# Kernel optimization log

Hardware: AMD Instinct MI355X
Metric: run time of the kernel (lower is better)

The kernel has to match this reference:

```python
import jax, jax.numpy as jnp
import numpy as np

B, N, D_IN, D_OUT = 4, 2048, 1024, 1024


def setup_inputs() -> dict:
    key = jax.random.key(0)
    k0, k1, k2, k3 = jax.random.split(key, 4)
    x = jax.random.normal(k0, (B, N, D_IN), dtype=jnp.float32)
    # torch Linear weight is [out, in]; store transposed [in, out] for x @ W
    W_query = jax.random.normal(k1, (D_IN, D_OUT), dtype=jnp.float32) * (D_IN ** -0.5)
    W_key = jax.random.normal(k2, (D_IN, D_OUT), dtype=jnp.float32) * (D_IN ** -0.5)
    W_value = jax.random.normal(k3, (D_IN, D_OUT), dtype=jnp.float32) * (D_IN ** -0.5)
    return {"x": x, "W_query": W_query, "W_key": W_key, "W_value": W_value}


def reference(x, W_query, W_key, W_value):
    # x: [B, N, D_IN]
    num_tokens = x.shape[1]
    embed_dim = x.shape[2]  # NB: original scales by INPUT embed dim
    q = jnp.einsum('bnd,de->bne', x, W_query)  # [B, N, D_OUT]
    k = jnp.einsum('bnd,de->bne', x, W_key)
    v = jnp.einsum('bnd,de->bne', x, W_value)
    scores = jnp.einsum('bqe,bke->bqk', q, k)  # [B, N, N]
    idx = jnp.arange(num_tokens)
    causal_mask = idx[None, :] > idx[:, None]  # True above diagonal
    scores = jnp.where(causal_mask[None, :, :], -jnp.inf, scores)
    scale = jnp.asarray(embed_dim, scores.dtype) ** 0.5
    attn = jax.nn.softmax(scores / scale, axis=-1)  # dropout p=0 (eval)
    context = jnp.einsum('bqk,bke->bqe', attn, v)  # [B, N, D_OUT]
    return context
```

## Files before the change

kernel.cpp:

```cpp
#include <hip/hip_runtime.h>


typedef __attribute__((ext_vector_type(8))) _Float16 half8;
typedef __attribute__((ext_vector_type(4))) _Float16 half4v;
typedef __attribute__((ext_vector_type(4))) float floatx4;

#define AS1 __attribute__((address_space(1)))
#define AS3 __attribute__((address_space(3)))

__device__ __forceinline__ void load16_lds(void* lds, const void* g) {
  __builtin_amdgcn_global_load_lds((AS1 void*)g, (AS3 void*)lds, 16, 0, 0);
}

__global__ __launch_bounds__(256)
void prep(const float* __restrict__ in, _Float16* __restrict__ out,
          const float* __restrict__ W0, const float* __restrict__ W1,
          const float* __restrict__ W2, _Float16* __restrict__ Wt) {
  const int bid = blockIdx.x;
  if (bid < 8192) {
    const int i = (bid * 256 + threadIdx.x) << 2;
    float4 v = *(const float4*)(in + i);
    half4v o = { (_Float16)v.x, (_Float16)v.y, (_Float16)v.z, (_Float16)v.w };
    *(half4v*)(out + i) = o;
  } else {
    const int t = bid - 8192;
    const int bz = t >> 10;
    const int rem = t & 1023;
    const int bx = rem & 31, by = rem >> 5;
    const float* W = bz == 0 ? W0 : (bz == 1 ? W1 : W2);
    _Float16* o = Wt + (long long)bz * 1048576;
    __shared__ _Float16 tl[32][33];
    const int tx = threadIdx.x & 31, ty = threadIdx.x >> 5;
    const int n0 = bx << 5, k0 = by << 5;
#pragma unroll
    for (int i = 0; i < 4; ++i)
      tl[ty + i * 8][tx] = (_Float16)W[(long long)(k0 + ty + i * 8) * 1024 + n0 + tx];
    __syncthreads();
#pragma unroll
    for (int i = 0; i < 4; ++i)
      o[(long long)(n0 + ty + i * 8) * 1024 + k0 + tx] = tl[tx][ty + i * 8];
  }
}

__global__ __launch_bounds__(256)
void gemm_qkv(const _Float16* __restrict__ A, const _Float16* __restrict__ B,
              _Float16* __restrict__ Q, _Float16* __restrict__ Kh,
              _Float16* __restrict__ Vt) {
  const int lid = blockIdx.x + 24 * blockIdx.y;
  const int swz = (lid & 7) * 192 + (lid >> 3);
  const int bm = swz / 24, bn = swz % 24;

  const _Float16* Ab = A + (long long)bm * 128 * 1024;
  const _Float16* Bb = B + (long long)bn * 128 * 1024;

  __shared__ _Float16 As[128][64];
  __shared__ _Float16 Bs[128][64];

  const int tid = threadIdx.x;
  const int wave = tid >> 6, lane = tid & 63;
  const int quad = lane >> 4, lr = lane & 15;
  const int wm = (wave >> 1) << 6, wn = (wave & 1) << 6;
  const int srow = lane >> 3;
  const int goff = ((lane & 7) ^ srow) << 3;

  floatx4 acc[4][4] = {};
  const _Float16* ga = Ab + (long long)(wave * 8 + srow) * 1024 + goff;
  const _Float16* gb = Bb + (long long)(wave * 8 + srow) * 1024 + goff;

  for (int k0 = 0; k0 < 1024; k0 += 64) {
    __syncthreads();
#pragma unroll
    for (int c = 0; c < 4; ++c) {
      load16_lds(&As[wave * 8 + 32 * c][0], ga + c * 32 * 1024);
      load16_lds(&Bs[wave * 8 + 32 * c][0], gb + c * 32 * 1024);
    }
    ga += 64; gb += 64;
    __syncthreads();

#pragma unroll
    for (int kk = 0; kk < 2; ++kk) {
      half8 af[4], bf[4];
#pragma unroll
      for (int i = 0; i < 4; ++i) {
        const int ra = wm + (i << 4) + lr;
        const int rb = wn + (i << 4) + lr;
        af[i] = *(const half8*)&As[ra][(((kk << 2) + quad) ^ (ra & 7)) << 3];
        bf[i] = *(const half8*)&Bs[rb][(((kk << 2) + quad) ^ (rb & 7)) << 3];
      }
#pragma unroll
      for (int i = 0; i < 4; ++i)
#pragma unroll
        for (int j = 0; j < 4; ++j)
          acc[i][j] = __builtin_amdgcn_mfma_f32_16x16x32_f16(af[i], bf[j], acc[i][j], 0, 0, 0);
    }
  }

  const int colb = bn * 128 + wn + lr;
  const int rowb = bm * 128 + wm + (quad << 2);

  if (bn < 16) {
    _Float16* C = (bn < 8) ? Q : Kh;
    const int cb = colb & 1023;
#pragma unroll
    for (int i = 0; i < 4; ++i)
#pragma unroll
      for (int j = 0; j < 4; ++j)
#pragma unroll
        for (int r = 0; r < 4; ++r)
          C[(long long)(rowb + (i << 4) + r) * 1024 + cb + (j << 4)] =
              (_Float16)acc[i][j][r];
  } else {
    const int b = rowb >> 11;
    const int tb = rowb & 2047;
#pragma unroll
    for (int i = 0; i < 4; ++i) {
      const int tok = tb + (i << 4);
#pragma unroll
      for (int j = 0; j < 4; ++j) {
        const int d = (colb & 1023) + (j << 4);
        half4v v = { (_Float16)acc[i][j][0], (_Float16)acc[i][j][1],
                     (_Float16)acc[i][j][2], (_Float16)acc[i][j][3] };
        *(half4v*)&Vt[(long long)b * 2097152 + (long long)d * 2048 + tok] = v;
      }
    }
  }
}

__global__ __launch_bounds__(256)
void gemm_s_exp(const _Float16* __restrict__ Q, const _Float16* __restrict__ Kh,
                _Float16* __restrict__ P, float* __restrict__ M,
                float* __restrict__ L) {
  int t = (blockIdx.x & 7) * 17 + (blockIdx.x >> 3);
  int bm = 0;
  for (;;) { const int c = bm + 1; if (t < c) break; t -= c; ++bm; }
  const int bn = t;
  const int bz = blockIdx.y;

  const _Float16* Ab = Q  + (long long)bz * 2097152 + (long long)bm * 128 * 1024;
  const _Float16* Bb = Kh + (long long)bz * 2097152 + (long long)bn * 128 * 1024;

  __shared__ _Float16 As[128][64];
  __shared__ _Float16 Bs[128][64];
  __shared__ float sm_m[2][2][64];
  __shared__ float sm_s[2][2][64];

  const int tid = threadIdx.x;
  const int wave = tid >> 6, lane = tid & 63;
  const int quad = lane >> 4, lr = lane & 15;
  const int wm = (wave >> 1) << 6, wn = (wave & 1) << 6;
  const int wm1 = wave >> 1, wn1 = wave & 1;
  const int srow = lane >> 3;
  const int schunk = lane & 7;
  const int goff = (schunk ^ srow) << 3;

  floatx4 acc[4][4] = {};
  const _Float16* ga = Ab + (long long)(wave * 8 + srow) * 1024 + goff;
  const _Float16* gb = Bb + (long long)(wave * 8 + srow) * 1024 + goff;

  half8 pa[4], pb[4];
#pragma unroll
  for (int c = 0; c < 4; ++c) {
    pa[c] = *(const half8*)(ga + c * 32 * 1024);
    pb[c] = *(const half8*)(gb + c * 32 * 1024);
  }

  for (int it = 0; it < 16; ++it) {
    __syncthreads();
#pragma unroll
    for (int c = 0; c < 4; ++c) {
      *(half8*)&As[wave * 8 + 32 * c + srow][schunk << 3] = pa[c];
      *(half8*)&Bs[wave * 8 + 32 * c + srow][schunk << 3] = pb[c];
    }
    __syncthreads();
    if (it + 1 < 16) {
      const int k1 = (it + 1) << 6;
#pragma unroll
      for (int c = 0; c < 4; ++c) {
        pa[c] = *(const half8*)(ga + c * 32 * 1024 + k1);
        pb[c] = *(const half8*)(gb + c * 32 * 1024 + k1);
      }
    }

#pragma unroll
    for (int kk = 0; kk < 2; ++kk) {
      half8 af[4], bf[4];
#pragma unroll
      for (int i = 0; i < 4; ++i) {
        const int ra = wm + (i << 4) + lr;
        const int rb = wn + (i << 4) + lr;
        af[i] = *(const half8*)&As[ra][(((kk << 2) + quad) ^ (ra & 7)) << 3];
        bf[i] = *(const half8*)&Bs[rb][(((kk << 2) + quad) ^ (rb & 7)) << 3];
      }
#pragma unroll
      for (int i = 0; i < 4; ++i)
#pragma unroll
        for (int j = 0; j < 4; ++j)
          acc[i][j] = __builtin_amdgcn_mfma_f32_16x16x32_f16(af[i], bf[j], acc[i][j], 0, 0, 0);
    }
  }

  const int colb = bn * 128 + wn + lr;
  const int rowb = bm * 128 + wm + (quad << 2);
  _Float16* Pb = P + (long long)bz * 4194304;
  const float scl = 0.03125f;

  float mx[4][4], rs[4][4];
#pragma unroll
  for (int i = 0; i < 4; ++i)
#pragma unroll
    for (int r = 0; r < 4; ++r) { mx[i][r] = -3.0e38f; rs[i][r] = 0.f; }

#pragma unroll
  for (int i = 0; i < 4; ++i)
#pragma unroll
    for (int j = 0; j < 4; ++j)
#pragma unroll
      for (int r = 0; r < 4; ++r) {
        const int qr = rowb + (i << 4) + r;
        const int kcol = colb + (j << 4);
        if (kcol <= qr) mx[i][r] = fmaxf(mx[i][r], acc[i][j][r] * scl);
      }
#pragma unroll
  for (int i = 0; i < 4; ++i)
#pragma unroll
    for (int r = 0; r < 4; ++r) {
#pragma unroll
      for (int off = 1; off < 16; off <<= 1)
        mx[i][r] = fmaxf(mx[i][r], __shfl_xor(mx[i][r], off));
    }

  if (lr == 0) {
#pragma unroll
    for (int i = 0; i < 4; ++i)
#pragma unroll
      for (int r = 0; r < 4; ++r)
        sm_m[wm1][wn1][(i << 4) + (quad << 2) + r] = mx[i][r];
  }
  __syncthreads();
  float mt[4][4];
#pragma unroll
  for (int i = 0; i < 4; ++i)
#pragma unroll
    for (int r = 0; r < 4; ++r)
      mt[i][r] = fmaxf(mx[i][r], sm_m[wm1][wn1 ^ 1][(i << 4) + (quad << 2) + r]);

#pragma unroll
  for (int i = 0; i < 4; ++i)
#pragma unroll
    for (int j = 0; j < 4; ++j)
#pragma unroll
      for (int r = 0; r < 4; ++r) {
        const int qr = rowb + (i << 4) + r;
        const int kcol = colb + (j << 4);
        const float pv =
            (kcol <= qr) ? __expf(acc[i][j][r] * scl - mt[i][r]) : 0.f;
        Pb[(long long)qr * 2048 + kcol] = (_Float16)pv;
        rs[i][r] += pv;
      }

#pragma unroll
  for (int i = 0; i < 4; ++i)
#pragma unroll
    for (int r = 0; r < 4; ++r) {
#pragma unroll
      for (int off = 1; off < 16; off <<= 1)
        rs[i][r] += __shfl_xor(rs[i][r], off);
    }

  if (lr == 0) {
#pragma unroll
    for (int i = 0; i < 4; ++i)
#pragma unroll
      for (int r = 0; r < 4; ++r)
        sm_s[wm1][wn1][(i << 4) + (quad << 2) + r] = rs[i][r];
  }
  __syncthreads();
  if (wn1 == 0 && lr == 0) {
    float* Mb = M + ((long long)bz * 16 + bn) * 2048;
    float* Lb = L + ((long long)bz * 16 + bn) * 2048;
#pragma unroll
    for (int i = 0; i < 4; ++i)
#pragma unroll
      for (int r = 0; r < 4; ++r) {
        const int lrow = (i << 4) + (quad << 2) + r;
        const int row = rowb + (i << 4) + r;
        Mb[row] = mt[i][r];
        Lb[row] = rs[i][r] + sm_s[wm1][1][lrow];
      }
  }
}

__global__ __launch_bounds__(256)
void combine(const float* __restrict__ M, const float* __restrict__ L,
             float* __restrict__ F, float* __restrict__ lg) {
  const int idx = blockIdx.x * 256 + threadIdx.x;
  const int bz = idx >> 11, row = idx & 2047;
  const int nt = (row >> 7) + 1;
  const float* Mb = M + (long long)bz * 32768;
  const float* Lb = L + (long long)bz * 32768;
  float* Fb = F + (long long)bz * 32768;

  float mg = -3.0e38f;
  for (int t = 0; t < nt; ++t) mg = fmaxf(mg, Mb[t * 2048 + row]);
  float s = 0.f;
  for (int t = 0; t < nt; ++t) {
    const float f = __expf(Mb[t * 2048 + row] - mg);
    Fb[t * 2048 + row] = f;
    s += f * Lb[t * 2048 + row];
  }
  lg[bz * 2048 + row] = s;
}

__global__ __launch_bounds__(256)
void gemm_pv(const _Float16* __restrict__ P, const _Float16* __restrict__ Vt,
             const float* __restrict__ F, const float* __restrict__ lg,
             float* __restrict__ out) {
  const int lid = blockIdx.x + (blockIdx.y << 3) + (blockIdx.z << 7);
  const int xcd = lid & 7, slot = lid >> 3;
  const int dn = slot & 7;
  const int p = slot >> 3;
  const int bz = p & 3;
  const int bm = (p >> 2) ? xcd : (15 - xcd);
  const int niter = 2 * (bm + 1);

  const _Float16* Ab = P  + (long long)bz * 4194304 + (long long)bm * 128 * 2048;
  const _Float16* Bb = Vt + (long long)bz * 2097152 + (long long)dn * 128 * 2048;
  const float* Fb = F + (long long)bz * 32768 + (long long)bm * 128;

  __shared__ _Float16 As[128][64];
  __shared__ _Float16 Bs[128][64];

  const int tid = threadIdx.x;
  const int wave = tid >> 6, lane = tid & 63;
  const int quad = lane >> 4, lr = lane & 15;
  const int wm = (wave >> 1) << 6, wn = (wave & 1) << 6;
  const int srow = lane >> 3;
  const int schunk = lane & 7;
  const int goff = (schunk ^ srow) << 3;
  const int lrow0 = wave * 8 + srow;

  floatx4 acc[4][4] = {};
  const _Float16* ga = Ab + (long long)lrow0 * 2048 + goff;
  const _Float16* gb = Bb + (long long)lrow0 * 2048 + goff;

  half8 pa[4], pb[4];
  float fr[4];
#pragma unroll
  for (int c = 0; c < 4; ++c) {
    pa[c] = *(const half8*)(ga + (long long)c * 32 * 2048);
    pb[c] = *(const half8*)(gb + (long long)c * 32 * 2048);
    fr[c] = Fb[lrow0 + 32 * c];
  }

  for (int it = 0; it < niter; ++it) {
    __syncthreads();
#pragma unroll
    for (int c = 0; c < 4; ++c) {
      *(half8*)&As[wave * 8 + 32 * c + srow][schunk << 3] =
          pa[c] * (_Float16)fr[c];
      *(half8*)&Bs[wave * 8 + 32 * c + srow][schunk << 3] = pb[c];
    }
    __syncthreads();
    if (it + 1 < niter) {
      const int k1 = (it + 1) << 6;
      const int kt1 = (it + 1) >> 1;
#pragma unroll
      for (int c = 0; c < 4; ++c) {
        pa[c] = *(const half8*)(ga + (long long)c * 32 * 2048 + k1);
        pb[c] = *(const half8*)(gb + (long long)c * 32 * 2048 + k1);
        fr[c] = Fb[kt1 * 2048 + lrow0 + 32 * c];
      }
    }

#pragma unroll
    for (int kk = 0; kk < 2; ++kk) {
      half8 af[4], bf[4];
#pragma unroll
      for (int i = 0; i < 4; ++i) {
        const int ra = wm + (i << 4) + lr;
        const int rb = wn + (i << 4) + lr;
        af[i] = *(const half8*)&As[ra][(((kk << 2) + quad) ^ (ra & 7)) << 3];
        bf[i] = *(const half8*)&Bs[rb][(((kk << 2) + quad) ^ (rb & 7)) << 3];
      }
#pragma unroll
      for (int i = 0; i < 4; ++i)
#pragma unroll
        for (int j = 0; j < 4; ++j)
          acc[i][j] = __builtin_amdgcn_mfma_f32_16x16x32_f16(af[i], bf[j], acc[i][j], 0, 0, 0);
    }
  }

  const int colb = dn * 128 + wn + lr;
  const int rowb = bm * 128 + wm + (quad << 2);
  const float* lb = lg + bz * 2048;
  float* Cb = out + (long long)bz * 2097152;

  float linv[4][4];
#pragma unroll
  for (int i = 0; i < 4; ++i)
#pragma unroll
    for (int r = 0; r < 4; ++r)
      linv[i][r] = 1.0f / lb[rowb + (i << 4) + r];

#pragma unroll
  for (int i = 0; i < 4; ++i)
#pragma unroll
    for (int j = 0; j < 4; ++j)
#pragma unroll
      for (int r = 0; r < 4; ++r)
        Cb[(long long)(rowb + (i << 4) + r) * 1024 + colb + (j << 4)] =
            acc[i][j][r] * linv[i][r];
}


extern "C" void kernel_launch(void* const* d_in, const int* in_sizes, int n_in,
                              void* d_out, int out_size, void* d_ws, size_t ws_size,
                              hipStream_t stream) {
  const float* x  = (const float*)d_in[0];
  const float* Wq = (const float*)d_in[1];
  const float* Wk = (const float*)d_in[2];
  const float* Wv = (const float*)d_in[3];
  float* out = (float*)d_out;

  char* ws = (char*)d_ws;
  _Float16* xh = (_Float16*)(ws);
  _Float16* Wt = (_Float16*)(ws + 16777216);
  _Float16* Q  = (_Float16*)(ws + 23068672);
  _Float16* Kh = (_Float16*)(ws + 39845888);
  _Float16* Vt = (_Float16*)(ws + 56623104);
  _Float16* P  = (_Float16*)(ws + 73400320);
  float*    M  = (float*)   (ws + 106954752);
  float*    L  = (float*)   (ws + 107479040);
  float*    F  = (float*)   (ws + 108003328);
  float*    lg = (float*)   (ws + 108527616);

  prep<<<11264, 256, 0, stream>>>(x, xh, Wq, Wk, Wv, Wt);

  gemm_qkv<<<dim3(24, 64), 256, 0, stream>>>(xh, Wt, Q, Kh, Vt);

  gemm_s_exp<<<dim3(136, 4), 256, 0, stream>>>(Q, Kh, P, M, L);

  combine<<<32, 256, 0, stream>>>(M, L, F, lg);

  gemm_pv<<<dim3(8, 16, 4), 256, 0, stream>>>(P, Vt, F, lg, out);
}
```

Baseline: 254.7 us.

## Fuse softmax combine into PV GEMM, swap operands for vectorized stores

```diff
diff --git a/kernel.cpp b/kernel.cpp
--- a/kernel.cpp
+++ b/kernel.cpp
@@ -46,10 +46,7 @@
 void gemm_qkv(const _Float16* __restrict__ A, const _Float16* __restrict__ B,
               _Float16* __restrict__ Q, _Float16* __restrict__ Kh,
               _Float16* __restrict__ Vt) {
-  const int lid = blockIdx.x + 24 * blockIdx.y;
-  const int swz = (lid & 7) * 192 + (lid >> 3);
-  const int bm = swz / 24, bn = swz % 24;
-
+  const int bm = blockIdx.y, bn = blockIdx.x;
   const _Float16* Ab = A + (long long)bm * 128 * 1024;
   const _Float16* Bb = B + (long long)bn * 128 * 1024;
 
@@ -291,44 +288,27 @@
 }
 
 __global__ __launch_bounds__(256)
-void combine(const float* __restrict__ M, const float* __restrict__ L,
-             float* __restrict__ F, float* __restrict__ lg) {
-  const int idx = blockIdx.x * 256 + threadIdx.x;
-  const int bz = idx >> 11, row = idx & 2047;
-  const int nt = (row >> 7) + 1;
-  const float* Mb = M + (long long)bz * 32768;
-  const float* Lb = L + (long long)bz * 32768;
-  float* Fb = F + (long long)bz * 32768;
-
-  float mg = -3.0e38f;
-  for (int t = 0; t < nt; ++t) mg = fmaxf(mg, Mb[t * 2048 + row]);
-  float s = 0.f;
-  for (int t = 0; t < nt; ++t) {
-    const float f = __expf(Mb[t * 2048 + row] - mg);
-    Fb[t * 2048 + row] = f;
-    s += f * Lb[t * 2048 + row];
-  }
-  lg[bz * 2048 + row] = s;
-}
-
-__global__ __launch_bounds__(256)
 void gemm_pv(const _Float16* __restrict__ P, const _Float16* __restrict__ Vt,
-             const float* __restrict__ F, const float* __restrict__ lg,
+             const float* __restrict__ M, const float* __restrict__ L,
              float* __restrict__ out) {
   const int lid = blockIdx.x + (blockIdx.y << 3) + (blockIdx.z << 7);
-  const int xcd = lid & 7, slot = lid >> 3;
-  const int dn = slot & 7;
-  const int p = slot >> 3;
-  const int bz = p & 3;
-  const int bm = (p >> 2) ? xcd : (15 - xcd);
+  const int xcd = lid & 7;
+  const int s = lid >> 3;
+  const int p = s >> 4;
+  const int dnl = (s >> 2) & 3;
+  const int bz = s & 3;
+  const int bmg = xcd >> 1, dng = xcd & 1;
+  const int bm = (p < 2) ? (15 - 2 * bmg - p) : (2 * bmg + (3 - p));
+  const int dn = dng * 4 + dnl;
   const int niter = 2 * (bm + 1);
 
-  const _Float16* Ab = P  + (long long)bz * 4194304 + (long long)bm * 128 * 2048;
-  const _Float16* Bb = Vt + (long long)bz * 2097152 + (long long)dn * 128 * 2048;
-  const float* Fb = F + (long long)bz * 32768 + (long long)bm * 128;
+  const _Float16* Ab = Vt + (long long)bz * 2097152 + (long long)dn * 128 * 2048;
+  const _Float16* Bb = P  + (long long)bz * 4194304 + (long long)bm * 128 * 2048;
 
   __shared__ _Float16 As[128][64];
   __shared__ _Float16 Bs[128][64];
+  __shared__ float F_lds[16][128];
+  __shared__ float linv_lds[128];
 
   const int tid = threadIdx.x;
   const int wave = tid >> 6, lane = tid & 63;
@@ -339,36 +319,47 @@
   const int goff = (schunk ^ srow) << 3;
   const int lrow0 = wave * 8 + srow;
 
+  if (tid < 128) {
+    const float* Mb = M + (long long)bz * 32768 + bm * 128 + tid;
+    const float* Lb = L + (long long)bz * 32768 + bm * 128 + tid;
+    float mg = -3.0e38f;
+    for (int t = 0; t <= bm; ++t) mg = fmaxf(mg, Mb[t * 2048]);
+    float ssum = 0.f;
+    for (int t = 0; t <= bm; ++t) {
+      const float f = __expf(Mb[t * 2048] - mg);
+      F_lds[t][tid] = f;
+      ssum += f * Lb[t * 2048];
+    }
+    linv_lds[tid] = 1.0f / ssum;
+  }
+
   floatx4 acc[4][4] = {};
   const _Float16* ga = Ab + (long long)lrow0 * 2048 + goff;
   const _Float16* gb = Bb + (long long)lrow0 * 2048 + goff;
 
   half8 pa[4], pb[4];
-  float fr[4];
 #pragma unroll
   for (int c = 0; c < 4; ++c) {
     pa[c] = *(const half8*)(ga + (long long)c * 32 * 2048);
     pb[c] = *(const half8*)(gb + (long long)c * 32 * 2048);
-    fr[c] = Fb[lrow0 + 32 * c];
   }
 
   for (int it = 0; it < niter; ++it) {
     __syncthreads();
+    const int kt = it >> 1;
 #pragma unroll
     for (int c = 0; c < 4; ++c) {
-      *(half8*)&As[wave * 8 + 32 * c + srow][schunk << 3] =
-          pa[c] * (_Float16)fr[c];
-      *(half8*)&Bs[wave * 8 + 32 * c + srow][schunk << 3] = pb[c];
+      *(half8*)&As[wave * 8 + 32 * c + srow][schunk << 3] = pa[c];
+      *(half8*)&Bs[wave * 8 + 32 * c + srow][schunk << 3] =
+          pb[c] * (_Float16)F_lds[kt][lrow0 + 32 * c];
     }
     __syncthreads();
     if (it + 1 < niter) {
       const int k1 = (it + 1) << 6;
-      const int kt1 = (it + 1) >> 1;
 #pragma unroll
       for (int c = 0; c < 4; ++c) {
         pa[c] = *(const half8*)(ga + (long long)c * 32 * 2048 + k1);
         pb[c] = *(const half8*)(gb + (long long)c * 32 * 2048 + k1);
-        fr[c] = Fb[kt1 * 2048 + lrow0 + 32 * c];
       }
     }
 
@@ -390,26 +381,22 @@
     }
   }
 
-  const int colb = dn * 128 + wn + lr;
-  const int rowb = bm * 128 + wm + (quad << 2);
-  const float* lb = lg + bz * 2048;
   float* Cb = out + (long long)bz * 2097152;
-
-  float linv[4][4];
-#pragma unroll
-  for (int i = 0; i < 4; ++i)
-#pragma unroll
-    for (int r = 0; r < 4; ++r)
-      linv[i][r] = 1.0f / lb[rowb + (i << 4) + r];
-
-#pragma unroll
-  for (int i = 0; i < 4; ++i)
-#pragma unroll
-    for (int j = 0; j < 4; ++j)
-#pragma unroll
-      for (int r = 0; r < 4; ++r)
-        Cb[(long long)(rowb + (i << 4) + r) * 1024 + colb + (j << 4)] =
-            acc[i][j][r] * linv[i][r];
+  const int d0 = dn * 128 + wm + (quad << 2);
+  const int q0 = bm * 128 + wn + lr;
+
+  float linv[4];
+#pragma unroll
+  for (int j = 0; j < 4; ++j) linv[j] = linv_lds[wn + (j << 4) + lr];
+
+#pragma unroll
+  for (int i = 0; i < 4; ++i)
+#pragma unroll
+    for (int j = 0; j < 4; ++j) {
+      float4 v = { acc[i][j][0] * linv[j], acc[i][j][1] * linv[j],
+                   acc[i][j][2] * linv[j], acc[i][j][3] * linv[j] };
+      *(float4*)&Cb[(long long)(q0 + (j << 4)) * 1024 + d0 + (i << 4)] = v;
+    }
 }
 
 
@@ -431,8 +418,6 @@
   _Float16* P  = (_Float16*)(ws + 73400320);
   float*    M  = (float*)   (ws + 106954752);
   float*    L  = (float*)   (ws + 107479040);
-  float*    F  = (float*)   (ws + 108003328);
-  float*    lg = (float*)   (ws + 108527616);
 
   prep<<<11264, 256, 0, stream>>>(x, xh, Wq, Wk, Wv, Wt);
 
@@ -440,7 +425,5 @@
 
   gemm_s_exp<<<dim3(136, 4), 256, 0, stream>>>(Q, Kh, P, M, L);
 
-  combine<<<32, 256, 0, stream>>>(M, L, F, lg);
-
-  gemm_pv<<<dim3(8, 16, 4), 256, 0, stream>>>(P, Vt, F, lg, out);
-}
+  gemm_pv<<<dim3(8, 16, 4), 256, 0, stream>>>(P, Vt, M, L, out);
+}
```

New measurement: 241.4 us. 1.06x faster.
